# Performance work log

Hardware: AMD Instinct MI355X
Metric: run time of the kernel (lower is better)

Reference implementation:

```python
import jax, jax.numpy as jnp
import numpy as np

N, E, D_IN, D_OUT = 100000, 1600000, 128, 128


def setup_inputs() -> dict:
    key = jax.random.key(0)
    k1, k2, k3, k4 = jax.random.split(key, 4)
    x = jax.random.normal(k1, (N, D_IN), dtype=jnp.float32)
    edge_index = jax.random.randint(k2, (2, E), 0, N, dtype=jnp.int64)
    # nn.Linear(in_feats, out_feats): W is (out, in) in torch; store (in, out) for x @ W
    bound = 1.0 / np.sqrt(D_IN)
    W = jax.random.uniform(k3, (D_IN, D_OUT), dtype=jnp.float32, minval=-bound, maxval=bound)
    b = jax.random.uniform(k4, (D_OUT,), dtype=jnp.float32, minval=-bound, maxval=bound)
    return {"x": x, "edge_index": edge_index, "W": W, "b": b}


def reference(x, edge_index, W, b):
    src, dst = edge_index[0], edge_index[1]
    # gather src features then scatter-sum into dst slots (dim_size=N)
    agg = jax.ops.segment_sum(x[src], dst, num_segments=N)  # (N, D_in)
    return agg @ W + b  # (N, D_out)
```

## Files before the change

### kernel.cpp

```cpp
#include <hip/hip_runtime.h>
#include <hip/hip_bf16.h>

#define D 128
#define GRP 64
#define NBMAX 4096
#define CAPB_MAX 2048

typedef __attribute__((ext_vector_type(8))) short short8;
typedef __attribute__((ext_vector_type(4))) float f32x4;

__device__ __forceinline__ float bf2f(unsigned short u) {
    union { unsigned int i; float f; } c;
    c.i = ((unsigned int)u) << 16;
    return c.f;
}
__device__ __forceinline__ float bits2f(unsigned int i) {
    union { unsigned int i; float f; } c;
    c.i = i;
    return c.f;
}
__device__ __forceinline__ unsigned short f2bf(float f) {
    __hip_bfloat16 h = __float2bfloat16(f);
    return *(unsigned short*)&h;
}

__global__ __launch_bounds__(64) void probe_kernel(
    const unsigned short* __restrict__ x,
    const long long* __restrict__ ei64,
    int nNodes, int* __restrict__ flags)
{
    const int lane = threadIdx.x;
    int cnt = 0;
    for (int i = lane; i < 512; i += 64) {
        float v = bf2f(x[i]);
        if (!(fabsf(v) < 1e4f)) cnt++;
    }
    unsigned long long m1 = __ballot(cnt > 0);
    long long v = ei64[lane];
    int bad = (v < 0 || v >= (long long)nNodes) ? 1 : 0;
    unsigned long long m2 = __ballot(bad);
    if (lane == 0) {
        flags[0] = (__popcll(m1) > 2) ? 1 : 0;
        flags[1] = (m2 == 0) ? 1 : 0;
    }
}

__global__ __launch_bounds__(256, 2) void gemm_mfma(
    const void* __restrict__ xv, const void* __restrict__ Wv, void* __restrict__ yv,
    int nNodes, int nTiles, const int* __restrict__ flags)
{
    __shared__ unsigned short Wth[D * D];
    __shared__ unsigned short Wtl[D * D];

    const int xf32 = flags[0];
    const int tid = threadIdx.x;
    const int w = tid >> 6, l = tid & 63;
    const int lr = l & 15, g = l >> 4;

    if (xf32) {
        const float* W = (const float*)Wv;
        for (int i = tid; i < D * D; i += 256) {
            int c = i & 127, k = i >> 7;
            float wv = W[(size_t)k * D + c];
            unsigned short hi = f2bf(wv);
            unsigned short lo = f2bf(wv - bf2f(hi));
            int ba = (((c << 7) + k) << 1) ^ ((c & 7) << 4);
            *(unsigned short*)((char*)Wth + ba) = hi;
            *(unsigned short*)((char*)Wtl + ba) = lo;
        }
    } else {
        const unsigned short* W = (const unsigned short*)Wv;
        for (int i = tid; i < D * D / 2; i += 256) {
            int c = i & 127, k2 = i >> 7;
            unsigned int v0 = W[(size_t)(2 * k2) * D + c];
            unsigned int v1 = W[(size_t)(2 * k2 + 1) * D + c];
            unsigned int pk = v0 | (v1 << 16);
            int ba = (((c << 7) + 2 * k2) << 1) ^ ((c & 7) << 4);
            *(unsigned int*)((char*)Wth + ba) = pk;
        }
    }
    __syncthreads();

    unsigned short* y = (unsigned short*)yv;

    for (int t = blockIdx.x; t < nTiles; t += gridDim.x) {
        const int row0 = t * 64 + w * 16;
        int arow = row0 + lr; if (arow >= nNodes) arow = nNodes - 1;

        short8 ah[4], al[4];
        if (xf32) {
            const float* xr = (const float*)xv + (size_t)arow * D;
            #pragma unroll
            for (int kk = 0; kk < 4; ++kk) {
                float f[8];
                *(float4*)&f[0] = *(const float4*)(xr + kk * 32 + g * 8);
                *(float4*)&f[4] = *(const float4*)(xr + kk * 32 + g * 8 + 4);
                #pragma unroll
                for (int i = 0; i < 8; ++i) {
                    unsigned short hi = f2bf(f[i]);
                    ah[kk][i] = (short)hi;
                    al[kk][i] = (short)f2bf(f[i] - bf2f(hi));
                }
            }
        } else {
            const char* xrow = (const char*)xv + (size_t)arow * (D * 2);
            #pragma unroll
            for (int kk = 0; kk < 4; ++kk)
                ah[kk] = *(const short8*)(xrow + (kk << 6) + (g << 4));
        }

        #pragma unroll
        for (int c = 0; c < 8; ++c) {
            const int col = c * 16 + lr;
            f32x4 acc = {0.f, 0.f, 0.f, 0.f};
            #pragma unroll
            for (int kk = 0; kk < 4; ++kk) {
                int ba = ((col << 8) + (kk << 6) + (g << 4)) ^ ((col & 7) << 4);
                short8 bh = *(const short8*)((const char*)Wth + ba);
                acc = __builtin_amdgcn_mfma_f32_16x16x32_bf16(ah[kk], bh, acc, 0, 0, 0);
                if (xf32) {
                    short8 bl = *(const short8*)((const char*)Wtl + ba);
                    acc = __builtin_amdgcn_mfma_f32_16x16x32_bf16(ah[kk], bl, acc, 0, 0, 0);
                    acc = __builtin_amdgcn_mfma_f32_16x16x32_bf16(al[kk], bh, acc, 0, 0, 0);
                }
            }
            #pragma unroll
            for (int j = 0; j < 4; ++j) {
                int row = row0 + g * 4 + j;
                if (row < nNodes)
                    y[(size_t)row * D + col] = f2bf(acc[j]);
            }
        }
    }
}

__global__ __launch_bounds__(256) void gemm_kernel(
    const void* __restrict__ inv, const void* __restrict__ Wv,
    const void* __restrict__ bv, void* __restrict__ outv,
    int nNodes, const int* __restrict__ flags,
    int in_f32p, int out_f32p, int add_bias)
{
    __shared__ float Ws[D * D];
    __shared__ float bs[D];

    const int xf32 = flags[0];
    const int in_f32  = (in_f32p  < 0) ? xf32 : in_f32p;
    const int out_f32 = (out_f32p < 0) ? xf32 : out_f32p;

    if (xf32) {
        const float* W = (const float*)Wv;
        for (int i = threadIdx.x; i < D * D; i += 256) Ws[i] = W[i];
        if (threadIdx.x < D)
            bs[threadIdx.x] = add_bias ? ((const float*)bv)[threadIdx.x] : 0.f;
    } else {
        const unsigned short* W = (const unsigned short*)Wv;
        for (int i = threadIdx.x; i < D * D; i += 256) Ws[i] = bf2f(W[i]);
        if (threadIdx.x < D)
            bs[threadIdx.x] = add_bias ? bf2f(((const unsigned short*)bv)[threadIdx.x]) : 0.f;
    }
    __syncthreads();

    const int cg = threadIdx.x & 31;
    const int rg = threadIdx.x >> 5;
    const int c = cg * 4;
    const int row0 = blockIdx.x * 64 + rg * 8;

    size_t rIdx[8];
    #pragma unroll
    for (int r = 0; r < 8; ++r) {
        int row = row0 + r;
        rIdx[r] = (size_t)(row < nNodes ? row : nNodes - 1);
    }

    float4 acc[8];
    #pragma unroll
    for (int r = 0; r < 8; ++r)
        acc[r] = make_float4(bs[c], bs[c + 1], bs[c + 2], bs[c + 3]);

    if (in_f32) {
        const float* in = (const float*)inv;
        for (int k = 0; k < D; k += 4) {
            float4 w0 = *(const float4*)&Ws[(k + 0) * D + c];
            float4 w1 = *(const float4*)&Ws[(k + 1) * D + c];
            float4 w2 = *(const float4*)&Ws[(k + 2) * D + c];
            float4 w3 = *(const float4*)&Ws[(k + 3) * D + c];
            #pragma unroll
            for (int r = 0; r < 8; ++r) {
                float4 a = *(const float4*)(in + rIdx[r] * D + k);
                acc[r].x += a.x * w0.x + a.y * w1.x + a.z * w2.x + a.w * w3.x;
                acc[r].y += a.x * w0.y + a.y * w1.y + a.z * w2.y + a.w * w3.y;
                acc[r].z += a.x * w0.z + a.y * w1.z + a.z * w2.z + a.w * w3.z;
                acc[r].w += a.x * w0.w + a.y * w1.w + a.z * w2.w + a.w * w3.w;
            }
        }
    } else {
        const unsigned short* in = (const unsigned short*)inv;
        for (int k = 0; k < D; k += 4) {
            float4 w0 = *(const float4*)&Ws[(k + 0) * D + c];
            float4 w1 = *(const float4*)&Ws[(k + 1) * D + c];
            float4 w2 = *(const float4*)&Ws[(k + 2) * D + c];
            float4 w3 = *(const float4*)&Ws[(k + 3) * D + c];
            #pragma unroll
            for (int r = 0; r < 8; ++r) {
                ushort4 u = *(const ushort4*)(in + rIdx[r] * D + k);
                float ax = bf2f(u.x), ay = bf2f(u.y), az = bf2f(u.z), aw = bf2f(u.w);
                acc[r].x += ax * w0.x + ay * w1.x + az * w2.x + aw * w3.x;
                acc[r].y += ax * w0.y + ay * w1.y + az * w2.y + aw * w3.y;
                acc[r].z += ax * w0.z + ay * w1.z + az * w2.z + aw * w3.z;
                acc[r].w += ax * w0.w + ay * w1.w + az * w2.w + aw * w3.w;
            }
        }
    }

    #pragma unroll
    for (int r = 0; r < 8; ++r) {
        int row = row0 + r;
        if (row >= nNodes) break;
        if (out_f32) {
            ((float4*)outv)[(size_t)row * 32 + cg] = acc[r];
        } else {
            ushort4 o;
            o.x = f2bf(acc[r].x); o.y = f2bf(acc[r].y);
            o.z = f2bf(acc[r].z); o.w = f2bf(acc[r].w);
            ((ushort4*)outv)[(size_t)row * 32 + cg] = o;
        }
    }
}

__global__ __launch_bounds__(256) void bin_edges(
    const void* __restrict__ eiv, int* __restrict__ gcnt, unsigned int* __restrict__ grp,
    int* __restrict__ ovfCnt, int* __restrict__ ovfHead, int2* __restrict__ ovf,
    int nEdges, int NB, int CAPB, int nPer, const int* __restrict__ flags)
{
    __shared__ int cnts[NBMAX];
    __shared__ int run[NBMAX];

    const int e0 = blockIdx.x * nPer;
    int e1 = e0 + nPer; if (e1 > nEdges) e1 = nEdges;
    const int i64 = flags[1];
    const long long* ei64 = (const long long*)eiv;
    const int* ei32 = (const int*)eiv;

    for (int i = threadIdx.x; i < NB; i += 256) cnts[i] = 0;
    __syncthreads();

    for (int e = e0 + threadIdx.x; e < e1; e += 256) {
        int d = i64 ? (int)ei64[(size_t)nEdges + e] : ei32[(size_t)nEdges + e];
        atomicAdd(&cnts[d >> 6], 1);
    }
    __syncthreads();

    for (int g = threadIdx.x; g < NB; g += 256) {
        int c = cnts[g];
        run[g] = (c > 0) ? atomicAdd(&gcnt[(size_t)g * 16], c) : 0;
    }
    __syncthreads();

    for (int e = e0 + threadIdx.x; e < e1; e += 256) {
        int s, d;
        if (i64) { s = (int)ei64[e]; d = (int)ei64[(size_t)nEdges + e]; }
        else     { s = ei32[e];      d = ei32[(size_t)nEdges + e]; }
        int g = d >> 6;
        int pos = atomicAdd(&run[g], 1);
        unsigned int p = (unsigned int)s | ((unsigned int)(d & 63) << 20);
        if (pos < CAPB) {
            grp[(size_t)g * CAPB + pos] = p;
        } else {
            int idx = atomicAdd(ovfCnt, 1);
            int old = atomicExch(&ovfHead[g], idx);
            ovf[idx] = make_int2(old, (int)p);
        }
    }
}

__global__ __launch_bounds__(256, 4) void sort_accum(
    const unsigned int* __restrict__ yu,
    const int* __restrict__ gcnt, const unsigned int* __restrict__ grp,
    const int* __restrict__ ovfHead, const int2* __restrict__ ovf,
    const void* __restrict__ bv, void* __restrict__ outv,
    int nNodes, int CAPB, const int* __restrict__ flags)
{
    __shared__ unsigned int sorted[CAPB_MAX];
    __shared__ int rcnt[GRP], roff[GRP], rrun[GRP];

    const int g = blockIdx.x;
    const int n0 = g << 6;
    const int tid = threadIdx.x;
    const int w = tid >> 6, lane = tid & 63;
    const int xf32 = flags[0];

    if (tid < GRP) rcnt[tid] = 0;
    __syncthreads();

    const int cnt = gcnt[(size_t)g * 16];
    const int m = cnt < CAPB ? cnt : CAPB;

    for (int i = tid; i < m; i += 256)
        atomicAdd(&rcnt[grp[(size_t)g * CAPB + i] >> 20], 1);
    __syncthreads();

    if (w == 0) {
        int v = rcnt[lane];
        int sc = v;
        #pragma unroll
        for (int o = 1; o < 64; o <<= 1) {
            int t = __shfl_up(sc, o);
            if (lane >= o) sc += t;
        }
        roff[lane] = sc - v;
        rrun[lane] = sc - v;
    }
    __syncthreads();

    for (int i = tid; i < m; i += 256) {
        unsigned int p = grp[(size_t)g * CAPB + i];
        int pos = atomicAdd(&rrun[p >> 20], 1);
        sorted[pos] = p & 0xFFFFFu;
    }
    __syncthreads();

    const bool hasOvf = (cnt > CAPB);

    for (int r = w; r < GRP; r += 4) {
        int node = n0 + r;
        if (node >= nNodes) break;
        const int j0 = roff[r], dg = rcnt[r];

        float a0 = 0.f, a1 = 0.f, a2 = 0.f, a3 = 0.f;
        float b0 = 0.f, b1 = 0.f, b2 = 0.f, b3 = 0.f;
        int j = 0;
        for (; j + 4 <= dg; j += 4) {
            unsigned int s0 = sorted[j0 + j + 0];
            unsigned int s1 = sorted[j0 + j + 1];
            unsigned int s2 = sorted[j0 + j + 2];
            unsigned int s3 = sorted[j0 + j + 3];
            unsigned int u0 = yu[(size_t)s0 * 64 + lane];
            unsigned int u1 = yu[(size_t)s1 * 64 + lane];
            unsigned int u2 = yu[(size_t)s2 * 64 + lane];
            unsigned int u3 = yu[(size_t)s3 * 64 + lane];
            a0 += bits2f(u0 << 16); b0 += bits2f(u0 & 0xFFFF0000u);
            a1 += bits2f(u1 << 16); b1 += bits2f(u1 & 0xFFFF0000u);
            a2 += bits2f(u2 << 16); b2 += bits2f(u2 & 0xFFFF0000u);
            a3 += bits2f(u3 << 16); b3 += bits2f(u3 & 0xFFFF0000u);
        }
        for (; j < dg; ++j) {
            unsigned int s0 = sorted[j0 + j];
            unsigned int u0 = yu[(size_t)s0 * 64 + lane];
            a0 += bits2f(u0 << 16); b0 += bits2f(u0 & 0xFFFF0000u);
        }

        if (hasOvf) {
            int cur = ovfHead[g];
            while (cur >= 0) {
                int2 t = ovf[cur];
                unsigned int p = (unsigned int)t.y;
                if ((int)(p >> 20) == r) {
                    unsigned int u = yu[(size_t)(p & 0xFFFFFu) * 64 + lane];
                    a0 += bits2f(u << 16); b0 += bits2f(u & 0xFFFF0000u);
                }
                cur = t.x;
            }
        }

        float f0 = (a0 + a1) + (a2 + a3);
        float f1 = (b0 + b1) + (b2 + b3);

        if (xf32) {
            float2 bb = ((const float2*)bv)[lane];
            float2 o; o.x = f0 + bb.x; o.y = f1 + bb.y;
            ((float2*)outv)[(size_t)node * 64 + lane] = o;
        } else {
            unsigned int ub = ((const unsigned int*)bv)[lane];
            f0 += bits2f(ub << 16);
            f1 += bits2f(ub & 0xFFFF0000u);
            unsigned int o = ((unsigned int)f2bf(f0)) | (((unsigned int)f2bf(f1)) << 16);
            ((unsigned int*)outv)[(size_t)node * 64 + lane] = o;
        }
    }
}

__global__ __launch_bounds__(256) void scatter_kernel(
    const void* __restrict__ xv, const void* __restrict__ eiv,
    float* __restrict__ agg, int nEdges, const int* __restrict__ flags)
{
    long long tid = (long long)blockIdx.x * 256 + threadIdx.x;
    int e = (int)(tid >> 5);
    if (e >= nEdges) return;
    int q = (int)tid & 31;

    const int xf32 = flags[0];
    int s, d;
    if (flags[1]) {
        const long long* ei = (const long long*)eiv;
        s = (int)ei[e]; d = (int)ei[(size_t)nEdges + e];
    } else {
        const int* ei = (const int*)eiv;
        s = ei[e]; d = ei[(size_t)nEdges + e];
    }
    float4 v;
    if (xf32) {
        v = ((const float4*)xv)[(size_t)s * 32 + q];
    } else {
        ushort4 u = ((const ushort4*)xv)[(size_t)s * 32 + q];
        v.x = bf2f(u.x); v.y = bf2f(u.y); v.z = bf2f(u.z); v.w = bf2f(u.w);
    }
    float* ap = agg + (size_t)d * D + q * 4;
    atomicAdd(ap + 0, v.x);
    atomicAdd(ap + 1, v.y);
    atomicAdd(ap + 2, v.z);
    atomicAdd(ap + 3, v.w);
}

static inline size_t alignup(size_t v, size_t a) { return (v + a - 1) & ~(a - 1); }

extern "C" void kernel_launch(void* const* d_in, const int* in_sizes, int n_in,
                              void* d_out, int out_size, void* d_ws, size_t ws_size,
                              hipStream_t stream) {
    const void* x  = d_in[0];
    const void* ei = d_in[1];
    const void* W  = d_in[2];
    const void* b  = d_in[3];

    const int nNodes = in_sizes[0] / D;
    const int nEdges = in_sizes[1] / 2;
    const int NB = (nNodes + GRP - 1) / GRP;

    int* flags = (int*)d_ws;
    probe_kernel<<<1, 64, 0, stream>>>((const unsigned short*)x, (const long long*)ei,
                                       nNodes, flags);

    int CAPB = 0;
    size_t off_gcnt = 512, off_ovfc = 0, off_head = 0, off_ovf = 0, off_grp = 0, off_y = 0;
    if (nNodes < (1 << 20) && NB <= NBMAX) {
        int cap = CAPB_MAX;
        size_t ogcnt = 512;
        size_t oovfc = alignup(ogcnt + 64ull * NB, 256);
        size_t ohead = oovfc + 256;
        size_t oovf  = alignup(ohead + 4ull * NB, 256);
        size_t ogrp  = alignup(oovf + 8ull * nEdges, 256);
        size_t oy    = alignup(ogrp + 4ull * cap * NB, 512);
        size_t need  = oy + (size_t)nNodes * D * 2;
        if (ws_size >= need) {
            CAPB = cap; off_gcnt = ogcnt; off_ovfc = oovfc; off_head = ohead;
            off_ovf = oovf; off_grp = ogrp; off_y = oy;
        }
    }

    const int mblocks = (nNodes + 63) / 64;

    if (CAPB > 0) {
        int*          gcnt    = (int*)((char*)d_ws + off_gcnt);
        int*          ovfCnt  = (int*)((char*)d_ws + off_ovfc);
        int*          ovfHead = (int*)((char*)d_ws + off_head);
        int2*         ovf     = (int2*)((char*)d_ws + off_ovf);
        unsigned int* grp     = (unsigned int*)((char*)d_ws + off_grp);
        void*         y       = (void*)((char*)d_ws + off_y);

        int gblocks = mblocks < 512 ? mblocks : 512;
        gemm_mfma<<<gblocks, 256, 0, stream>>>(x, W, y, nNodes, mblocks, flags);

        hipMemsetAsync(gcnt, 0, off_head - off_gcnt, stream);
        hipMemsetAsync(ovfHead, 0xFF, 4ull * NB, stream);

        const int ABLK = 256;
        const int nPer = (nEdges + ABLK - 1) / ABLK;
        bin_edges<<<ABLK, 256, 0, stream>>>(ei, gcnt, grp, ovfCnt, ovfHead, ovf,
                                            nEdges, NB, CAPB, nPer, flags);

        sort_accum<<<NB, 256, 0, stream>>>((const unsigned int*)y, gcnt, grp,
                                           ovfHead, ovf, b, d_out,
                                           nNodes, CAPB, flags);
    } else {
        float* agg = (float*)((char*)d_ws + 512);
        hipMemsetAsync(agg, 0, (size_t)nNodes * D * sizeof(float), stream);
        long long total = (long long)nEdges * 32;
        int sblocks = (int)((total + 255) / 256);
        scatter_kernel<<<sblocks, 256, 0, stream>>>(x, ei, agg, nEdges, flags);
        gemm_kernel<<<mblocks, 256, 0, stream>>>(agg, W, b, d_out, nNodes, flags,
                                                 1, -1, 1);
    }
}
```

Baseline: 246.5 us.

## Fold probe and memsets into kernels, unroll gather loop by eight

```diff
diff --git a/kernel.cpp b/kernel.cpp
--- a/kernel.cpp
+++ b/kernel.cpp
@@ -22,6 +22,35 @@
 __device__ __forceinline__ unsigned short f2bf(float f) {
     __hip_bfloat16 h = __float2bfloat16(f);
     return *(unsigned short*)&h;
+}
+
+__device__ __forceinline__ int block_probe_xf32(const unsigned short* x) {
+    __shared__ int cntS;
+    if (threadIdx.x == 0) cntS = 0;
+    __syncthreads();
+    int bad = 0;
+    for (int i = threadIdx.x; i < 512; i += blockDim.x) {
+        float v = bf2f(x[i]);
+        if (!(fabsf(v) < 1e4f)) bad++;
+    }
+    if (bad) atomicAdd(&cntS, bad);
+    __syncthreads();
+    int r = (cntS > 2) ? 1 : 0;
+    __syncthreads();
+    return r;
+}
+__device__ __forceinline__ int block_probe_i64(const void* eiv, int nNodes) {
+    __shared__ int okS;
+    if (threadIdx.x == 0) okS = 1;
+    __syncthreads();
+    if (threadIdx.x < 64) {
+        long long v = ((const long long*)eiv)[threadIdx.x];
+        if (v < 0 || v >= (long long)nNodes) atomicAnd(&okS, 0);
+    }
+    __syncthreads();
+    int r = okS;
+    __syncthreads();
+    return r;
 }
 
 __global__ __launch_bounds__(64) void probe_kernel(
@@ -47,13 +76,18 @@
 
 __global__ __launch_bounds__(256, 2) void gemm_mfma(
     const void* __restrict__ xv, const void* __restrict__ Wv, void* __restrict__ yv,
-    int nNodes, int nTiles, const int* __restrict__ flags)
+    int nNodes, int nTiles,
+    int* __restrict__ zbase, int zInts, int* __restrict__ mhead, int NB)
 {
     __shared__ unsigned short Wth[D * D];
     __shared__ unsigned short Wtl[D * D];
 
-    const int xf32 = flags[0];
     const int tid = threadIdx.x;
+
+    for (int i = blockIdx.x * 256 + tid; i < zInts; i += gridDim.x * 256) zbase[i] = 0;
+    for (int i = blockIdx.x * 256 + tid; i < NB; i += gridDim.x * 256) mhead[i] = -1;
+
+    const int xf32 = block_probe_xf32((const unsigned short*)xv);
     const int w = tid >> 6, l = tid & 63;
     const int lr = l & 15, g = l >> 4;
 
@@ -230,14 +264,15 @@
 __global__ __launch_bounds__(256) void bin_edges(
     const void* __restrict__ eiv, int* __restrict__ gcnt, unsigned int* __restrict__ grp,
     int* __restrict__ ovfCnt, int* __restrict__ ovfHead, int2* __restrict__ ovf,
-    int nEdges, int NB, int CAPB, int nPer, const int* __restrict__ flags)
+    int nEdges, int nNodes, int NB, int CAPB, int nPer)
 {
     __shared__ int cnts[NBMAX];
     __shared__ int run[NBMAX];
 
+    const int i64 = block_probe_i64(eiv, nNodes);
+
     const int e0 = blockIdx.x * nPer;
     int e1 = e0 + nPer; if (e1 > nEdges) e1 = nEdges;
-    const int i64 = flags[1];
     const long long* ei64 = (const long long*)eiv;
     const int* ei32 = (const int*)eiv;
 
@@ -274,20 +309,22 @@
 }
 
 __global__ __launch_bounds__(256, 4) void sort_accum(
+    const void* __restrict__ xv,
     const unsigned int* __restrict__ yu,
     const int* __restrict__ gcnt, const unsigned int* __restrict__ grp,
     const int* __restrict__ ovfHead, const int2* __restrict__ ovf,
     const void* __restrict__ bv, void* __restrict__ outv,
-    int nNodes, int CAPB, const int* __restrict__ flags)
+    int nNodes, int CAPB)
 {
     __shared__ unsigned int sorted[CAPB_MAX];
     __shared__ int rcnt[GRP], roff[GRP], rrun[GRP];
+
+    const int xf32 = block_probe_xf32((const unsigned short*)xv);
 
     const int g = blockIdx.x;
     const int n0 = g << 6;
     const int tid = threadIdx.x;
     const int w = tid >> 6, lane = tid & 63;
-    const int xf32 = flags[0];
 
     if (tid < GRP) rcnt[tid] = 0;
     __syncthreads();
@@ -329,6 +366,18 @@
         float a0 = 0.f, a1 = 0.f, a2 = 0.f, a3 = 0.f;
         float b0 = 0.f, b1 = 0.f, b2 = 0.f, b3 = 0.f;
         int j = 0;
+        for (; j + 8 <= dg; j += 8) {
+            unsigned int s[8], u[8];
+            #pragma unroll
+            for (int t = 0; t < 8; ++t) s[t] = sorted[j0 + j + t];
+            #pragma unroll
+            for (int t = 0; t < 8; ++t) u[t] = yu[(size_t)s[t] * 64 + lane];
+            #pragma unroll
+            for (int t = 0; t < 8; ++t) {
+                if (t & 1) { a1 += bits2f(u[t] << 16); b1 += bits2f(u[t] & 0xFFFF0000u); }
+                else       { a0 += bits2f(u[t] << 16); b0 += bits2f(u[t] & 0xFFFF0000u); }
+            }
+        }
         for (; j + 4 <= dg; j += 4) {
             unsigned int s0 = sorted[j0 + j + 0];
             unsigned int s1 = sorted[j0 + j + 1];
@@ -424,10 +473,6 @@
     const int nNodes = in_sizes[0] / D;
     const int nEdges = in_sizes[1] / 2;
     const int NB = (nNodes + GRP - 1) / GRP;
-
-    int* flags = (int*)d_ws;
-    probe_kernel<<<1, 64, 0, stream>>>((const unsigned short*)x, (const long long*)ei,
-                                       nNodes, flags);
 
     int CAPB = 0;
     size_t off_gcnt = 512, off_ovfc = 0, off_head = 0, off_ovf = 0, off_grp = 0, off_y = 0;
@@ -455,22 +500,26 @@
         int2*         ovf     = (int2*)((char*)d_ws + off_ovf);
         unsigned int* grp     = (unsigned int*)((char*)d_ws + off_grp);
         void*         y       = (void*)((char*)d_ws + off_y);
+        (void)ovfCnt;
+
+        const int zInts = (int)((off_head - off_gcnt) / 4);
 
         int gblocks = mblocks < 512 ? mblocks : 512;
-        gemm_mfma<<<gblocks, 256, 0, stream>>>(x, W, y, nNodes, mblocks, flags);
-
-        hipMemsetAsync(gcnt, 0, off_head - off_gcnt, stream);
-        hipMemsetAsync(ovfHead, 0xFF, 4ull * NB, stream);
+        gemm_mfma<<<gblocks, 256, 0, stream>>>(x, W, y, nNodes, mblocks,
+                                               gcnt, zInts, ovfHead, NB);
 
         const int ABLK = 256;
         const int nPer = (nEdges + ABLK - 1) / ABLK;
         bin_edges<<<ABLK, 256, 0, stream>>>(ei, gcnt, grp, ovfCnt, ovfHead, ovf,
-                                            nEdges, NB, CAPB, nPer, flags);
-
-        sort_accum<<<NB, 256, 0, stream>>>((const unsigned int*)y, gcnt, grp,
+                                            nEdges, nNodes, NB, CAPB, nPer);
+
+        sort_accum<<<NB, 256, 0, stream>>>(x, (const unsigned int*)y, gcnt, grp,
                                            ovfHead, ovf, b, d_out,
-                                           nNodes, CAPB, flags);
+                                           nNodes, CAPB);
     } else {
+        int* flags = (int*)d_ws;
+        probe_kernel<<<1, 64, 0, stream>>>((const unsigned short*)x, (const long long*)ei,
+                                           nNodes, flags);
         float* agg = (float*)((char*)d_ws + 512);
         hipMemsetAsync(agg, 0, (size_t)nNodes * D * sizeof(float), stream);
         long long total = (long long)nEdges * 32;
```

Result: no change. 241.7 us (-2.0%).
